# Performance work log

Hardware: AMD Instinct MI355X
Metric: run time of the kernel (lower is better)

The kernel has to match this reference:

```python
import jax, jax.numpy as jnp
import numpy as np

B, T, DIM = 2, 2048, 1024
H, HKV, D = 16, 4, 64
ROPE_DIMS = 32
ROPE_BASE = 10000.0


def fake_quant(w, n_bits):
    # per-output-row absmax symmetric fake quantization with STE
    half = 2 ** (n_bits - 1)
    w_max = jnp.maximum(jnp.max(jnp.abs(w), axis=1, keepdims=True), 1e-5)
    w_int = jnp.clip(jnp.round(w / w_max * half), -half, half - 1)
    w_q = w_int / half * w_max
    return w + jax.lax.stop_gradient(w_q - w)


def rms_norm(x):
    eps = jnp.finfo(x.dtype).eps
    return x * jax.lax.rsqrt(jnp.mean(x * x, axis=-1, keepdims=True) + eps)


def rope_tables(seq_len, dtype):
    inv_freq = 1.0 / (ROPE_BASE ** (jnp.arange(0, ROPE_DIMS, 2, dtype=jnp.float32) / ROPE_DIMS))
    t = jnp.arange(seq_len, dtype=jnp.float32)
    freqs = t[:, None] * inv_freq[None, :]  # [T, rope_dims/2]
    return jnp.cos(freqs).astype(dtype)[None, None], jnp.sin(freqs).astype(dtype)[None, None]


def apply_rotary(x, cos, sin):
    # partial rotary: rotate first ROPE_DIMS dims, pass the rest through
    x_rope, x_pass = x[..., :ROPE_DIMS], x[..., ROPE_DIMS:]
    half = ROPE_DIMS // 2
    x1, x2 = x_rope[..., :half], x_rope[..., half:]
    rot = jnp.concatenate([x1 * cos + x2 * sin, -x1 * sin + x2 * cos], axis=-1)
    return jnp.concatenate([rot, x_pass], axis=-1)


def setup_inputs() -> dict:
    key = jax.random.key(0)
    ks = jax.random.split(key, 5)
    kv_dim = HKV * D
    return {
        "x": jax.random.normal(ks[0], (B, T, DIM), dtype=jnp.float32),
        "w_q": jax.random.normal(ks[1], (DIM, DIM), dtype=jnp.float32) * 0.02,
        "w_k": jax.random.normal(ks[2], (kv_dim, DIM), dtype=jnp.float32) * 0.02,
        "w_v": jax.random.normal(ks[3], (kv_dim, DIM), dtype=jnp.float32) * 0.02,
        "w_proj": jax.random.normal(ks[4], (DIM, DIM), dtype=jnp.float32) * 0.02,
        "q_gain": jnp.full((H,), 1.5, dtype=jnp.float32),
    }


def reference(x, w_q, w_k, w_v, w_proj, q_gain):
    bsz, seqlen, dim = x.shape
    group = H // HKV

    # quantized (STE) projections
    q = x @ fake_quant(w_q, 6).T        # [B, T, DIM]
    k = x @ fake_quant(w_k, 6).T        # [B, T, HKV*D]
    v = x @ fake_quant(w_v, 5).T        # [B, T, HKV*D]

    q = q.reshape(bsz, seqlen, H, D).transpose(0, 2, 1, 3)    # [B, H, T, D]
    k = k.reshape(bsz, seqlen, HKV, D).transpose(0, 2, 1, 3)  # [B, HKV, T, D]
    v = v.reshape(bsz, seqlen, HKV, D).transpose(0, 2, 1, 3)  # [B, HKV, T, D]

    q = rms_norm(q)
    k = rms_norm(k)

    cos, sin = rope_tables(seqlen, q.dtype)
    q = apply_rotary(q, cos, sin)
    k = apply_rotary(k, cos, sin)

    q = q * q_gain.astype(q.dtype)[None, :, None, None]

    # grouped-query causal attention; scores kept in grouped [B,HKV,g,T,T] layout
    qg = q.reshape(bsz, HKV, group, seqlen, D)
    scores = jnp.einsum('bhgqd,bhkd->bhgqk', qg, k) / jnp.sqrt(jnp.asarray(D, q.dtype))
    causal = jnp.tril(jnp.ones((seqlen, seqlen), dtype=bool))
    scores = jnp.where(causal[None, None, None], scores, jnp.asarray(-jnp.inf, scores.dtype))
    att = jax.nn.softmax(scores, axis=-1)
    y = jnp.einsum('bhgqk,bhkd->bhgqd', att, v)               # [B, HKV, g, T, D]

    # xsa: orthogonalize y against normalized v (per kv head group)
    y_g = y.transpose(0, 3, 1, 2, 4)                           # [B, T, HKV, g, D]
    v_t = v.transpose(0, 2, 1, 3)                              # [B, T, HKV, D]
    vn = v_t / jnp.maximum(jnp.linalg.norm(v_t, axis=-1, keepdims=True), 1e-12)
    vn = vn[..., None, :]                                      # [B, T, HKV, 1, D]
    proj = jnp.sum(y_g * vn, axis=-1, keepdims=True) * vn
    y_out = (y_g - proj).reshape(bsz, seqlen, dim)

    return y_out @ fake_quant(w_proj, 5).T
```

## Files before the change

### kernel.cpp

```cpp
#include <hip/hip_runtime.h>
#include <hip/hip_bf16.h>
#include <math.h>

typedef unsigned short u16;
typedef __attribute__((ext_vector_type(8))) short short8;
typedef __attribute__((ext_vector_type(4))) float float4v;
typedef __attribute__((ext_vector_type(4))) u16 ushort4v;

namespace {
constexpr int kT    = 2048;
constexpr int kDim  = 1024;
constexpr int kH    = 16;
constexpr int kHKV  = 4;
constexpr int kD    = 64;
constexpr int kTok  = 4096;
}

__device__ __forceinline__ u16 f2bf(float f) {
  unsigned int u = __builtin_bit_cast(unsigned int, f);
  u = (u + 0x7FFFu + ((u >> 16) & 1u)) >> 16;
  return (u16)u;
}
__device__ __forceinline__ unsigned pk2(float a, float b) {
  __hip_bfloat162 h = __float22bfloat162_rn(make_float2(a, b));
  unsigned u; __builtin_memcpy(&u, &h, 4);
  return u;
}
__device__ __forceinline__ uint2 pack4(float a, float b, float c, float d) {
  return make_uint2(pk2(a, b), pk2(c, d));
}

__device__ __forceinline__ void gl_lds16(const u16* g, u16* l) {
  __builtin_amdgcn_global_load_lds(
      (const __attribute__((address_space(1))) void*)g,
      (__attribute__((address_space(3))) void*)l, 16, 0, 0);
}

__global__ __launch_bounds__(256) void prep_kernel(
    const float* __restrict__ x,
    const float* __restrict__ w_q, const float* __restrict__ w_k,
    const float* __restrict__ w_v, const float* __restrict__ w_proj,
    u16* __restrict__ xb, u16* __restrict__ wqkv, u16* __restrict__ wpq,
    float2* __restrict__ ropetab)
{
  __shared__ float red[4];
  const int bid = blockIdx.x, tid = threadIdx.x;

  if (bid < 128) {
    const int idx = bid * 256 + tid;
    const int t = idx >> 4, i = idx & 15;
    const float fr = (float)t * powf(10000.0f, -(float)i * (1.0f / 16.0f));
    ropetab[idx] = make_float2(cosf(fr), sinf(fr));
    return;
  }
  if (bid < 2176) {
    const size_t i = ((size_t)(bid - 128) * 256 + tid) * 8;
    const float4 a = *(const float4*)(x + i);
    const float4 b = *(const float4*)(x + i + 4);
    short8 r;
    r[0] = (short)f2bf(a.x); r[1] = (short)f2bf(a.y);
    r[2] = (short)f2bf(a.z); r[3] = (short)f2bf(a.w);
    r[4] = (short)f2bf(b.x); r[5] = (short)f2bf(b.y);
    r[6] = (short)f2bf(b.z); r[7] = (short)f2bf(b.w);
    *(short8*)(xb + i) = r;
    return;
  }
  const int rid = bid - 2176;
  const float* src; u16* dst; float halfv;
  if (rid < 1024)      { src = w_q    + (size_t)rid * 1024;          dst = wqkv + (size_t)rid * 1024;          halfv = 32.0f; }
  else if (rid < 1280) { src = w_k    + (size_t)(rid - 1024) * 1024; dst = wqkv + (size_t)rid * 1024;          halfv = 32.0f; }
  else if (rid < 1536) { src = w_v    + (size_t)(rid - 1280) * 1024; dst = wqkv + (size_t)rid * 1024;          halfv = 16.0f; }
  else                 { src = w_proj + (size_t)(rid - 1536) * 1024; dst = wpq  + (size_t)(rid - 1536) * 1024; halfv = 16.0f; }

  const float4 v4 = *(const float4*)(src + tid * 4);
  float mx = fmaxf(fmaxf(fabsf(v4.x), fabsf(v4.y)), fmaxf(fabsf(v4.z), fabsf(v4.w)));
  #pragma unroll
  for (int m = 1; m < 64; m <<= 1) mx = fmaxf(mx, __shfl_xor(mx, m));
  if ((tid & 63) == 0) red[tid >> 6] = mx;
  __syncthreads();
  mx = fmaxf(fmaxf(red[0], red[1]), fmaxf(red[2], red[3]));
  const float wmax = fmaxf(mx, 1e-5f);
  const float inv_half = 1.0f / halfv;
  const float vals[4] = {v4.x, v4.y, v4.z, v4.w};
  ushort4v o;
  #pragma unroll
  for (int j = 0; j < 4; ++j) {
    float r = rintf(vals[j] / wmax * halfv);
    r = fminf(fmaxf(r, -halfv), halfv - 1.0f);
    o[j] = f2bf(r * inv_half * wmax);
  }
  *(ushort4v*)(dst + tid * 4) = o;
}

#define GEMM_GL_CORE(A_, W_, K_, NROW0_)                                       \
  __shared__ u16 As[128][64];                                                  \
  __shared__ u16 Bs[64][64];                                                   \
  const int tid = threadIdx.x;                                                 \
  const int lane = tid & 63, wv = tid >> 6;                                    \
  const int n = lane & 15, quad = lane >> 4;                                   \
  const int wm = wv * 32;                                                      \
  const int m0 = blockIdx.y * 128;                                             \
  const int lr8 = lane >> 3, lc8 = (lane & 7) * 8;                             \
  const u16* gA = A_ + (size_t)(m0 + wv * 32 + lr8) * K_ + lc8;                \
  const u16* gB = W_ + (size_t)(NROW0_ + wv * 16 + lr8) * K_ + lc8;            \
  float4v acc[2][4];                                                           \
  _Pragma("unroll")                                                            \
  for (int mi = 0; mi < 2; ++mi)                                               \
    _Pragma("unroll")                                                          \
    for (int ni = 0; ni < 4; ++ni) {                                           \
      acc[mi][ni][0]=0.f; acc[mi][ni][1]=0.f;                                  \
      acc[mi][ni][2]=0.f; acc[mi][ni][3]=0.f; }                                \
  for (int k0 = 0; k0 < K_; k0 += 64) {                                        \
    __syncthreads();                                                           \
    _Pragma("unroll")                                                          \
    for (int j = 0; j < 4; ++j)                                                \
      gl_lds16(gA + (size_t)(j * 8) * K_ + k0, &As[wv * 32 + j * 8][0]);       \
    _Pragma("unroll")                                                          \
    for (int j = 0; j < 2; ++j)                                                \
      gl_lds16(gB + (size_t)(j * 8) * K_ + k0, &Bs[wv * 16 + j * 8][0]);       \
    __syncthreads();                 \
    _Pragma("unroll")                                                          \
    for (int kk = 0; kk < 2; ++kk) {                                           \
      short8 af[2], bfr[4];                                                    \
      _Pragma("unroll")                                                        \
      for (int mi = 0; mi < 2; ++mi)                                           \
        af[mi] = *(const short8*)&As[wm + mi * 16 + n][kk * 32 + quad * 8];    \
      _Pragma("unroll")                                                        \
      for (int ni = 0; ni < 4; ++ni)                                           \
        bfr[ni] = *(const short8*)&Bs[ni * 16 + n][kk * 32 + quad * 8];        \
      _Pragma("unroll")                                                        \
      for (int mi = 0; mi < 2; ++mi)                                           \
        _Pragma("unroll")                                                      \
        for (int ni = 0; ni < 4; ++ni)                                         \
          acc[mi][ni] = __builtin_amdgcn_mfma_f32_16x16x32_bf16(af[mi], bfr[ni], acc[mi][ni], 0, 0, 0); \
    }                                                                          \
  }

__global__ __launch_bounds__(256) void gemm_qkv(
    const u16* __restrict__ A, const u16* __restrict__ W,
    const float2* __restrict__ ropetab, const float* __restrict__ q_gain,
    u16* __restrict__ qh, u16* __restrict__ kh,
    u16* __restrict__ vT, float* __restrict__ vcmp)
{
  GEMM_GL_CORE(A, W, kDim, (int)(blockIdx.x * 64))

  const int p = blockIdx.x;
  const int rbase = m0 + wm;
  const int bI = rbase >> 11;

  if (p < 20) {
    const float gain = (p < 16) ? q_gain[p] * 0.125f : 1.0f;
    u16* dst = (p < 16) ? qh + ((size_t)(bI * kH + p) * kT) * kD
                        : kh + ((size_t)(bI * kHKV + (p - 16)) * kT) * kD;
    #pragma unroll
    for (int mi = 0; mi < 2; ++mi)
      #pragma unroll
      for (int i = 0; i < 4; ++i) {
        const int row = rbase + mi * 16 + quad * 4 + i;
        const int t = row & (kT - 1);
        float v[4];
        #pragma unroll
        for (int ni = 0; ni < 4; ++ni) v[ni] = acc[mi][ni][i];
        float ss = v[0]*v[0] + v[1]*v[1] + v[2]*v[2] + v[3]*v[3];
        #pragma unroll
        for (int m = 1; m < 16; m <<= 1) ss += __shfl_xor(ss, m);
        const float rr = 1.0f / sqrtf(ss * (1.0f / 64.0f) + 1.1920929e-7f);
        #pragma unroll
        for (int ni = 0; ni < 4; ++ni) v[ni] *= rr;
        const float2 cs = ropetab[t * 16 + n];
        const float r0 =  v[0] * cs.x + v[1] * cs.y;
        const float r1 = -v[0] * cs.y + v[1] * cs.x;
        v[0] = r0; v[1] = r1;
        #pragma unroll
        for (int ni = 0; ni < 4; ++ni)
          dst[(size_t)t * kD + ni * 16 + n] = f2bf(v[ni] * gain);
      }
  } else {
    const int kvh = p - 20;
    u16* vTb = vT + ((size_t)(bI * kHKV + kvh) * kD) * kT;
    #pragma unroll
    for (int mi = 0; mi < 2; ++mi) {
      const int t0 = (rbase + mi * 16 + quad * 4) & (kT - 1);
      #pragma unroll
      for (int ni = 0; ni < 4; ++ni) {
        const int d = ni * 16 + n;
        *(uint2*)(vTb + (size_t)d * kT + t0) =
            pack4(acc[mi][ni][0], acc[mi][ni][1], acc[mi][ni][2], acc[mi][ni][3]);
        #pragma unroll
        for (int i = 0; i < 4; ++i)
          vcmp[(size_t)(rbase + mi * 16 + quad * 4 + i) * (kHKV * kD) + kvh * kD + d] = acc[mi][ni][i];
      }
    }
  }
}

__global__ __launch_bounds__(256) void gemm_out(
    const u16* __restrict__ A, const u16* __restrict__ W,
    float* __restrict__ C)
{
  GEMM_GL_CORE(A, W, kDim, (int)(blockIdx.x * 64))
  const int n0 = blockIdx.x * 64;
  #pragma unroll
  for (int mi = 0; mi < 2; ++mi)
    #pragma unroll
    for (int ni = 0; ni < 4; ++ni)
      #pragma unroll
      for (int i = 0; i < 4; ++i)
        C[(size_t)(m0 + wm + mi * 16 + quad * 4 + i) * kDim + n0 + ni * 16 + n] = acc[mi][ni][i];
}

__global__ __launch_bounds__(256) void attn_mfma(
    const u16* __restrict__ qh, const u16* __restrict__ kh,
    const u16* __restrict__ vT, const float* __restrict__ vcmp,
    u16* __restrict__ yo)
{
  __shared__ u16 ks[64][64];
  __shared__ u16 vs[64][64];
  __shared__ u16 ps[4][16][64];

  const int tid = threadIdx.x;
  const int lane = tid & 63, wq = tid >> 6;
  const int n = lane & 15, quad = lane >> 4;
  const int p = blockIdx.x;
  const int h = blockIdx.y, b = blockIdx.z;
  const int kv = h >> 2;
  const int tiles[2] = {p, 31 - p};
  const u16* kbase = kh + ((size_t)(b * kHKV + kv) * kT) * kD;
  const u16* vbase = vT + ((size_t)(b * kHKV + kv) * kD) * kT;

  short8 qa[2][2];
  {
    const u16* qb = qh + ((size_t)(b * kH + h) * kT) * kD;
    #pragma unroll
    for (int u = 0; u < 2; ++u) {
      const size_t row = (size_t)(tiles[u] * 64 + wq * 16 + n) * kD;
      qa[u][0] = *(const short8*)(qb + row + quad * 8);
      qa[u][1] = *(const short8*)(qb + row + 32 + quad * 8);
    }
  }

  const int sr = tid >> 3;
  const int sc = (tid & 7) * 8;
  const int scs = sc ^ ((sr & 7) * 8);

  float l_r[2] = {0.0f, 0.0f};
  float4v acc[2][4];
  #pragma unroll
  for (int u = 0; u < 2; ++u)
    #pragma unroll
    for (int g = 0; g < 4; ++g) { acc[u][g][0]=0.f; acc[u][g][1]=0.f; acc[u][g][2]=0.f; acc[u][g][3]=0.f; }

  short8 kr0, kr1, vr0, vr1;
  auto loadKV = [&](int kt) {
    kr0 = *(const short8*)(kbase + (size_t)(kt * 64 + sr) * kD + sc);
    kr1 = *(const short8*)(kbase + (size_t)(kt * 64 + sr + 32) * kD + sc);
    vr0 = *(const short8*)(vbase + (size_t)sr * kT + kt * 64 + sc);
    vr1 = *(const short8*)(vbase + (size_t)(sr + 32) * kT + kt * 64 + sc);
  };

  auto process = [&](int u, int kt) {
    float4v s[4];
    #pragma unroll
    for (int g = 0; g < 4; ++g) { s[g][0]=0.f; s[g][1]=0.f; s[g][2]=0.f; s[g][3]=0.f; }
    #pragma unroll
    for (int g = 0; g < 4; ++g) {
      const short8 kb0 = *(const short8*)&ks[g * 16 + n][(quad * 8) ^ ((n & 7) * 8)];
      s[g] = __builtin_amdgcn_mfma_f32_16x16x32_bf16(kb0, qa[u][0], s[g], 0, 0, 0);
      const short8 kb1 = *(const short8*)&ks[g * 16 + n][(32 + quad * 8) ^ ((n & 7) * 8)];
      s[g] = __builtin_amdgcn_mfma_f32_16x16x32_bf16(kb1, qa[u][1], s[g], 0, 0, 0);
    }
    if (kt == tiles[u]) {
      const int mloc = wq * 16 + n;
      #pragma unroll
      for (int g = 0; g < 4; ++g)
        #pragma unroll
        for (int i = 0; i < 4; ++i)
          if (g * 16 + quad * 4 + i > mloc) s[g][i] = -__builtin_inff();
    }
    float pf[4][4]; float rs = 0.0f;
    #pragma unroll
    for (int g = 0; g < 4; ++g)
      #pragma unroll
      for (int i = 0; i < 4; ++i) { pf[g][i] = __expf(s[g][i] - 12.0f); rs += pf[g][i]; }
    rs += __shfl_xor(rs, 16);
    rs += __shfl_xor(rs, 32);
    l_r[u] += rs;
    #pragma unroll
    for (int g = 0; g < 4; ++g)
      *(uint2*)&ps[wq][n][(g * 16 + quad * 4) ^ ((n & 7) * 8)] =
          pack4(pf[g][0], pf[g][1], pf[g][2], pf[g][3]);
    const short8 pb0 = *(const short8*)&ps[wq][n][(quad * 8) ^ ((n & 7) * 8)];
    const short8 pb1 = *(const short8*)&ps[wq][n][(32 + quad * 8) ^ ((n & 7) * 8)];
    #pragma unroll
    for (int g = 0; g < 4; ++g) {
      const short8 vb0 = *(const short8*)&vs[g * 16 + n][(quad * 8) ^ ((n & 7) * 8)];
      acc[u][g] = __builtin_amdgcn_mfma_f32_16x16x32_bf16(vb0, pb0, acc[u][g], 0, 0, 0);
      const short8 vb1 = *(const short8*)&vs[g * 16 + n][(32 + quad * 8) ^ ((n & 7) * 8)];
      acc[u][g] = __builtin_amdgcn_mfma_f32_16x16x32_bf16(vb1, pb1, acc[u][g], 0, 0, 0);
    }
  };

  const int kmax = tiles[1];
  loadKV(0);
  for (int kt = 0; kt <= kmax; ++kt) {
    __syncthreads();
    *(short8*)&ks[sr][scs]      = kr0;
    *(short8*)&ks[sr + 32][scs] = kr1;
    *(short8*)&vs[sr][scs]      = vr0;
    *(short8*)&vs[sr + 32][scs] = vr1;
    __syncthreads();
    if (kt < kmax) loadKV(kt + 1);
    process(1, kt);
    if (kt <= tiles[0]) process(0, kt);
  }

  #pragma unroll
  for (int u = 0; u < 2; ++u) {
    const int tok = b * kT + tiles[u] * 64 + wq * 16 + n;
    const float invl = 1.0f / l_r[u];
    float4 vv[4]; float nn = 0.0f, syr = 0.0f;
    #pragma unroll
    for (int g = 0; g < 4; ++g) {
      vv[g] = *(const float4*)(vcmp + (size_t)tok * (kHKV * kD) + kv * kD + g * 16 + quad * 4);
      nn  += vv[g].x * vv[g].x + vv[g].y * vv[g].y + vv[g].z * vv[g].z + vv[g].w * vv[g].w;
      syr += acc[u][g][0] * vv[g].x + acc[u][g][1] * vv[g].y + acc[u][g][2] * vv[g].z + acc[u][g][3] * vv[g].w;
    }
    nn  += __shfl_xor(nn, 16);  nn  += __shfl_xor(nn, 32);
    syr += __shfl_xor(syr, 16); syr += __shfl_xor(syr, 32);
    const float inv = 1.0f / fmaxf(sqrtf(nn), 1e-12f);
    const float coef = syr * invl * inv * inv;
    #pragma unroll
    for (int g = 0; g < 4; ++g)
      *(uint2*)(yo + (size_t)tok * kDim + h * kD + g * 16 + quad * 4) =
          pack4(acc[u][g][0] * invl - coef * vv[g].x,
                acc[u][g][1] * invl - coef * vv[g].y,
                acc[u][g][2] * invl - coef * vv[g].z,
                acc[u][g][3] * invl - coef * vv[g].w);
  }
}

extern "C" void kernel_launch(void* const* d_in, const int* in_sizes, int n_in,
                              void* d_out, int out_size, void* d_ws, size_t ws_size,
                              hipStream_t stream) {
  (void)in_sizes; (void)n_in; (void)out_size; (void)ws_size;
  const float* x      = (const float*)d_in[0];
  const float* w_q    = (const float*)d_in[1];
  const float* w_k    = (const float*)d_in[2];
  const float* w_v    = (const float*)d_in[3];
  const float* w_proj = (const float*)d_in[4];
  const float* q_gain = (const float*)d_in[5];

  char* wsb = (char*)d_ws;
  u16* wqkv = (u16*)wsb;  wsb += (size_t)1536 * 1024 * 2;
  u16* wpq  = (u16*)wsb;  wsb += (size_t)1024 * 1024 * 2;
  u16* xb   = (u16*)wsb;  wsb += (size_t)kTok * kDim * 2;
  u16* qh   = (u16*)wsb;  wsb += (size_t)kTok * kDim * 2;
  u16* khb  = (u16*)wsb;  wsb += (size_t)kTok * kHKV * kD * 2;
  u16* vTb  = (u16*)wsb;  wsb += (size_t)kTok * kHKV * kD * 2;
  u16* yo   = (u16*)wsb;  wsb += (size_t)kTok * kDim * 2;
  float* vcmp = (float*)wsb; wsb += (size_t)kTok * kHKV * kD * 4;
  float2* ropetab = (float2*)wsb; wsb += (size_t)kT * 16 * sizeof(float2);

  prep_kernel<<<4736, 256, 0, stream>>>(x, w_q, w_k, w_v, w_proj,
                                        xb, wqkv, wpq, ropetab);

  gemm_qkv<<<dim3(24, 32), 256, 0, stream>>>(xb, wqkv, ropetab, q_gain,
                                             qh, khb, vTb, vcmp);

  attn_mfma<<<dim3(16, kH, 2), 256, 0, stream>>>(qh, khb, vTb, vcmp, yo);

  gemm_out<<<dim3(16, 32), 256, 0, stream>>>(yo, wpq, (float*)d_out);
}
```

Measured before the change: 167.7 us.

## Split paired causal query tiles into one tile per block, heaviest first

Each attention block previously handled two query tiles (p and 31-p), balancing causal work and sharing each K/V tile load between both. Now each block handles a single query tile, with blocks ordered so the longest tiles launch first, doubling the grid to 1024 blocks. The aim is more parallelism and occupancy (fewer registers with one accumulator set) at the cost of loading each K/V tile twice as often and relying on the scheduler for load balance.

```diff
diff --git a/kernel.cpp b/kernel.cpp
--- a/kernel.cpp
+++ b/kernel.cpp
@@ -221,34 +221,28 @@
   const int tid = threadIdx.x;
   const int lane = tid & 63, wq = tid >> 6;
   const int n = lane & 15, quad = lane >> 4;
-  const int p = blockIdx.x;
+  const int qt = 31 - blockIdx.x;
   const int h = blockIdx.y, b = blockIdx.z;
   const int kv = h >> 2;
-  const int tiles[2] = {p, 31 - p};
   const u16* kbase = kh + ((size_t)(b * kHKV + kv) * kT) * kD;
   const u16* vbase = vT + ((size_t)(b * kHKV + kv) * kD) * kT;
 
-  short8 qa[2][2];
+  short8 qa0, qa1;
   {
     const u16* qb = qh + ((size_t)(b * kH + h) * kT) * kD;
-    #pragma unroll
-    for (int u = 0; u < 2; ++u) {
-      const size_t row = (size_t)(tiles[u] * 64 + wq * 16 + n) * kD;
-      qa[u][0] = *(const short8*)(qb + row + quad * 8);
-      qa[u][1] = *(const short8*)(qb + row + 32 + quad * 8);
-    }
+    const size_t row = (size_t)(qt * 64 + wq * 16 + n) * kD;
+    qa0 = *(const short8*)(qb + row + quad * 8);
+    qa1 = *(const short8*)(qb + row + 32 + quad * 8);
   }
 
   const int sr = tid >> 3;
   const int sc = (tid & 7) * 8;
   const int scs = sc ^ ((sr & 7) * 8);
 
-  float l_r[2] = {0.0f, 0.0f};
-  float4v acc[2][4];
+  float l_r = 0.0f;
+  float4v acc[4];
   #pragma unroll
-  for (int u = 0; u < 2; ++u)
-    #pragma unroll
-    for (int g = 0; g < 4; ++g) { acc[u][g][0]=0.f; acc[u][g][1]=0.f; acc[u][g][2]=0.f; acc[u][g][3]=0.f; }
+  for (int g = 0; g < 4; ++g) { acc[g][0]=0.f; acc[g][1]=0.f; acc[g][2]=0.f; acc[g][3]=0.f; }
 
   short8 kr0, kr1, vr0, vr1;
   auto loadKV = [&](int kt) {
@@ -258,72 +252,66 @@
     vr1 = *(const short8*)(vbase + (size_t)(sr + 32) * kT + kt * 64 + sc);
   };
 
-  auto process = [&](int u, int kt) {
-    float4v s[4];
-    #pragma unroll
-    for (int g = 0; g < 4; ++g) { s[g][0]=0.f; s[g][1]=0.f; s[g][2]=0.f; s[g][3]=0.f; }
-    #pragma unroll
-    for (int g = 0; g < 4; ++g) {
-      const short8 kb0 = *(const short8*)&ks[g * 16 + n][(quad * 8) ^ ((n & 7) * 8)];
-      s[g] = __builtin_amdgcn_mfma_f32_16x16x32_bf16(kb0, qa[u][0], s[g], 0, 0, 0);
-      const short8 kb1 = *(const short8*)&ks[g * 16 + n][(32 + quad * 8) ^ ((n & 7) * 8)];
-      s[g] = __builtin_amdgcn_mfma_f32_16x16x32_bf16(kb1, qa[u][1], s[g], 0, 0, 0);
-    }
-    if (kt == tiles[u]) {
-      const int mloc = wq * 16 + n;
-      #pragma unroll
-      for (int g = 0; g < 4; ++g)
-        #pragma unroll
-        for (int i = 0; i < 4; ++i)
-          if (g * 16 + quad * 4 + i > mloc) s[g][i] = -__builtin_inff();
-    }
-    float pf[4][4]; float rs = 0.0f;
-    #pragma unroll
-    for (int g = 0; g < 4; ++g)
-      #pragma unroll
-      for (int i = 0; i < 4; ++i) { pf[g][i] = __expf(s[g][i] - 12.0f); rs += pf[g][i]; }
-    rs += __shfl_xor(rs, 16);
-    rs += __shfl_xor(rs, 32);
-    l_r[u] += rs;
-    #pragma unroll
-    for (int g = 0; g < 4; ++g)
-      *(uint2*)&ps[wq][n][(g * 16 + quad * 4) ^ ((n & 7) * 8)] =
-          pack4(pf[g][0], pf[g][1], pf[g][2], pf[g][3]);
-    const short8 pb0 = *(const short8*)&ps[wq][n][(quad * 8) ^ ((n & 7) * 8)];
-    const short8 pb1 = *(const short8*)&ps[wq][n][(32 + quad * 8) ^ ((n & 7) * 8)];
-    #pragma unroll
-    for (int g = 0; g < 4; ++g) {
-      const short8 vb0 = *(const short8*)&vs[g * 16 + n][(quad * 8) ^ ((n & 7) * 8)];
-      acc[u][g] = __builtin_amdgcn_mfma_f32_16x16x32_bf16(vb0, pb0, acc[u][g], 0, 0, 0);
-      const short8 vb1 = *(const short8*)&vs[g * 16 + n][(32 + quad * 8) ^ ((n & 7) * 8)];
-      acc[u][g] = __builtin_amdgcn_mfma_f32_16x16x32_bf16(vb1, pb1, acc[u][g], 0, 0, 0);
-    }
-  };
-
-  const int kmax = tiles[1];
   loadKV(0);
-  for (int kt = 0; kt <= kmax; ++kt) {
+  for (int kt = 0; kt <= qt; ++kt) {
     __syncthreads();
     *(short8*)&ks[sr][scs]      = kr0;
     *(short8*)&ks[sr + 32][scs] = kr1;
     *(short8*)&vs[sr][scs]      = vr0;
     *(short8*)&vs[sr + 32][scs] = vr1;
     __syncthreads();
-    if (kt < kmax) loadKV(kt + 1);
-    process(1, kt);
-    if (kt <= tiles[0]) process(0, kt);
-  }
-
-  #pragma unroll
-  for (int u = 0; u < 2; ++u) {
-    const int tok = b * kT + tiles[u] * 64 + wq * 16 + n;
-    const float invl = 1.0f / l_r[u];
+    if (kt < qt) loadKV(kt + 1);
+
+    float4v s[4];
+    #pragma unroll
+    for (int g = 0; g < 4; ++g) { s[g][0]=0.f; s[g][1]=0.f; s[g][2]=0.f; s[g][3]=0.f; }
+    #pragma unroll
+    for (int g = 0; g < 4; ++g) {
+      const short8 kb0 = *(const short8*)&ks[g * 16 + n][(quad * 8) ^ ((n & 7) * 8)];
+      s[g] = __builtin_amdgcn_mfma_f32_16x16x32_bf16(kb0, qa0, s[g], 0, 0, 0);
+      const short8 kb1 = *(const short8*)&ks[g * 16 + n][(32 + quad * 8) ^ ((n & 7) * 8)];
+      s[g] = __builtin_amdgcn_mfma_f32_16x16x32_bf16(kb1, qa1, s[g], 0, 0, 0);
+    }
+    if (kt == qt) {
+      const int mloc = wq * 16 + n;
+      #pragma unroll
+      for (int g = 0; g < 4; ++g)
+        #pragma unroll
+        for (int i = 0; i < 4; ++i)
+          if (g * 16 + quad * 4 + i > mloc) s[g][i] = -__builtin_inff();
+    }
+    float pf[4][4]; float rs = 0.0f;
+    #pragma unroll
+    for (int g = 0; g < 4; ++g)
+      #pragma unroll
+      for (int i = 0; i < 4; ++i) { pf[g][i] = __expf(s[g][i] - 12.0f); rs += pf[g][i]; }
+    rs += __shfl_xor(rs, 16);
+    rs += __shfl_xor(rs, 32);
+    l_r += rs;
+    #pragma unroll
+    for (int g = 0; g < 4; ++g)
+      *(uint2*)&ps[wq][n][(g * 16 + quad * 4) ^ ((n & 7) * 8)] =
+          pack4(pf[g][0], pf[g][1], pf[g][2], pf[g][3]);
+    const short8 pb0 = *(const short8*)&ps[wq][n][(quad * 8) ^ ((n & 7) * 8)];
+    const short8 pb1 = *(const short8*)&ps[wq][n][(32 + quad * 8) ^ ((n & 7) * 8)];
+    #pragma unroll
+    for (int g = 0; g < 4; ++g) {
+      const short8 vb0 = *(const short8*)&vs[g * 16 + n][(quad * 8) ^ ((n & 7) * 8)];
+      acc[g] = __builtin_amdgcn_mfma_f32_16x16x32_bf16(vb0, pb0, acc[g], 0, 0, 0);
+      const short8 vb1 = *(const short8*)&vs[g * 16 + n][(32 + quad * 8) ^ ((n & 7) * 8)];
+      acc[g] = __builtin_amdgcn_mfma_f32_16x16x32_bf16(vb1, pb1, acc[g], 0, 0, 0);
+    }
+  }
+
+  {
+    const int tok = b * kT + qt * 64 + wq * 16 + n;
+    const float invl = 1.0f / l_r;
     float4 vv[4]; float nn = 0.0f, syr = 0.0f;
     #pragma unroll
     for (int g = 0; g < 4; ++g) {
       vv[g] = *(const float4*)(vcmp + (size_t)tok * (kHKV * kD) + kv * kD + g * 16 + quad * 4);
       nn  += vv[g].x * vv[g].x + vv[g].y * vv[g].y + vv[g].z * vv[g].z + vv[g].w * vv[g].w;
-      syr += acc[u][g][0] * vv[g].x + acc[u][g][1] * vv[g].y + acc[u][g][2] * vv[g].z + acc[u][g][3] * vv[g].w;
+      syr += acc[g][0] * vv[g].x + acc[g][1] * vv[g].y + acc[g][2] * vv[g].z + acc[g][3] * vv[g].w;
     }
     nn  += __shfl_xor(nn, 16);  nn  += __shfl_xor(nn, 32);
     syr += __shfl_xor(syr, 16); syr += __shfl_xor(syr, 32);
@@ -332,10 +320,10 @@
     #pragma unroll
     for (int g = 0; g < 4; ++g)
       *(uint2*)(yo + (size_t)tok * kDim + h * kD + g * 16 + quad * 4) =
-          pack4(acc[u][g][0] * invl - coef * vv[g].x,
-                acc[u][g][1] * invl - coef * vv[g].y,
-                acc[u][g][2] * invl - coef * vv[g].z,
-                acc[u][g][3] * invl - coef * vv[g].w);
+          pack4(acc[g][0] * invl - coef * vv[g].x,
+                acc[g][1] * invl - coef * vv[g].y,
+                acc[g][2] * invl - coef * vv[g].z,
+                acc[g][3] * invl - coef * vv[g].w);
   }
 }
 
@@ -367,7 +355,7 @@
   gemm_qkv<<<dim3(24, 32), 256, 0, stream>>>(xb, wqkv, ropetab, q_gain,
                                              qh, khb, vTb, vcmp);
 
-  attn_mfma<<<dim3(16, kH, 2), 256, 0, stream>>>(qh, khb, vTb, vcmp, yo);
+  attn_mfma<<<dim3(32, kH, 2), 256, 0, stream>>>(qh, khb, vTb, vcmp, yo);
 
   gemm_out<<<dim3(16, 32), 256, 0, stream>>>(yo, wpq, (float*)d_out);
 }
```

After: 186.1 us. +11.0%, slower.
